# Optimization experiments

Hardware: AMD Instinct MI355X
Metric: run time of the kernel (lower is better)

The kernel has to match this reference:

```python
import jax, jax.numpy as jnp
import numpy as np

N_NODES = 50000
N_EDGES = 800000
NEG_SLOPE = 0.2


def gat_conv(x, W, al, ar, b, src, dst, num_nodes):
    # x: [N, Din]; W: [Din, H*Dout]; al/ar: [H, Dout]; b: [H*Dout]
    H, Dout = al.shape
    h = (x @ W).reshape(num_nodes, H, Dout)            # [N, H, Dout]
    el = jnp.sum(h * al[None], axis=-1)                # [N, H]
    er = jnp.sum(h * ar[None], axis=-1)                # [N, H]
    e = jax.nn.leaky_relu(el[src] + er[dst], NEG_SLOPE)  # [E, H]
    # segment softmax over incoming edges of each dst node
    m = jax.ops.segment_max(e, dst, num_segments=num_nodes)
    m = jnp.where(jnp.isfinite(m), m, 0.0)
    ex = jnp.exp(e - m[dst])                           # [E, H]
    s = jax.ops.segment_sum(ex, dst, num_segments=num_nodes)
    alpha = ex / s[dst]                                # [E, H]
    msg = h[src] * alpha[:, :, None]                   # [E, H, Dout]
    out = jax.ops.segment_sum(msg, dst, num_segments=num_nodes)
    return out + b.reshape(1, H, Dout)                 # [N, H, Dout]


def setup_inputs() -> dict:
    key = jax.random.key(0)
    ks = jax.random.split(key, 12)
    d_in, hid, heads = 128, 128, 2
    inp = {
        "embedding": jax.random.normal(ks[0], (N_NODES, d_in), jnp.float32),
        "W0": jax.random.normal(ks[1], (d_in, heads * hid), jnp.float32) * 0.1,
        "al0": jax.random.normal(ks[2], (heads, hid), jnp.float32) * 0.1,
        "ar0": jax.random.normal(ks[3], (heads, hid), jnp.float32) * 0.1,
        "b0": jnp.zeros((heads * hid,), jnp.float32),
        "W1": jax.random.normal(ks[4], (heads * hid, heads * hid), jnp.float32) * 0.1,
        "al1": jax.random.normal(ks[5], (1, heads * hid), jnp.float32) * 0.1,
        "ar1": jax.random.normal(ks[6], (1, heads * hid), jnp.float32) * 0.1,
        "b1": jnp.zeros((heads * hid,), jnp.float32),
        "src": jax.random.randint(ks[7], (N_EDGES,), 0, N_NODES, jnp.int32),
        "dst": jax.random.randint(ks[8], (N_EDGES,), 0, N_NODES, jnp.int32),
    }
    return inp


def reference(embedding, W0, al0, ar0, b0, W1, al1, ar1, b1, src, dst):
    n = embedding.shape[0]
    # layer 0: 2 heads, then flatten heads and ReLU (dropout no-op in eval)
    x = gat_conv(embedding, W0, al0, ar0, b0, src, dst, n)  # [N, 2, 128]
    x = jax.nn.relu(x.reshape(n, -1))                        # [N, 256]
    # layer 1: 1 head, squeeze
    x = gat_conv(x, W1, al1, ar1, b1, src, dst, n)           # [N, 1, 256]
    x = x.reshape(n, -1)
    x = x.at[0].set(0.0)
    return x
```

## Files before the change

### kernel.cpp

```cpp
#include <hip/hip_runtime.h>


typedef __attribute__((ext_vector_type(8))) short short8v;
typedef __attribute__((ext_vector_type(4))) float f32x4;

__device__ inline unsigned short f2bf(float x) {
    union { float f; unsigned int u; } v; v.f = x;
    unsigned int r = v.u + 0x7fffu + ((v.u >> 16) & 1u);
    return (unsigned short)(r >> 16);
}
__device__ inline float bf2f(unsigned short h) {
    union { unsigned int u; float f; } v; v.u = ((unsigned int)h) << 16;
    return v.f;
}

__global__ void convW(const float* __restrict__ W, unsigned short* __restrict__ Wt,
                      int K, int N)
{
    int t = blockIdx.x * blockDim.x + threadIdx.x;
    if (t < K * N) {
        int k = t / N, n2 = t - k * N;
        Wt[n2 * K + k] = f2bf(W[t]);
    }
}

template<int AFP32, int H>
__global__ __launch_bounds__(256) void gemm_fused(
    const void* __restrict__ Av, const unsigned short* __restrict__ Bt,
    unsigned short* __restrict__ C,
    const float* __restrict__ al, const float* __restrict__ ar,
    float* __restrict__ el, float* __restrict__ er,
    int M, int N, int K)
{
    __shared__ __align__(16) unsigned short As[128 * 64];
    __shared__ __align__(16) unsigned short Bs[64 * 64];
    const int tid = threadIdx.x;
    const int lane = tid & 63, wv = tid >> 6;
    const int rowBase = blockIdx.x * 128;
    const int colBase = blockIdx.y * 64;

    f32x4 acc[2][4];
    #pragma unroll
    for (int i = 0; i < 2; ++i)
        #pragma unroll
        for (int j = 0; j < 4; ++j)
            acc[i][j] = (f32x4){0.f, 0.f, 0.f, 0.f};

    for (int k0 = 0; k0 < K; k0 += 64) {
        #pragma unroll
        for (int c = tid; c < 128 * 8; c += 256) {
            int row = c >> 3, cc = c & 7;
            int gr = rowBase + row; if (gr >= M) gr = M - 1;
            unsigned short* dstp = &As[row * 64 + (cc ^ (row & 7)) * 8];
            if (AFP32) {
                const float* A = (const float*)Av;
                const float* ap = A + (size_t)gr * K + k0 + cc * 8;
                float4 v0 = *(const float4*)ap;
                float4 v1 = *(const float4*)(ap + 4);
                ushort4 o0, o1;
                o0.x = f2bf(v0.x); o0.y = f2bf(v0.y); o0.z = f2bf(v0.z); o0.w = f2bf(v0.w);
                o1.x = f2bf(v1.x); o1.y = f2bf(v1.y); o1.z = f2bf(v1.z); o1.w = f2bf(v1.w);
                *(ushort4*)dstp = o0;
                *(ushort4*)(dstp + 4) = o1;
            } else {
                const unsigned short* A = (const unsigned short*)Av;
                int4 v = *(const int4*)(A + (size_t)gr * K + k0 + cc * 8);
                *(int4*)dstp = v;
            }
        }
        #pragma unroll
        for (int c = tid; c < 64 * 8; c += 256) {
            int n2 = c >> 3, cc = c & 7;
            int4 v = *(const int4*)(Bt + (size_t)(colBase + n2) * K + k0 + cc * 8);
            *(int4*)&Bs[n2 * 64 + (cc ^ (n2 & 7)) * 8] = v;
        }
        __syncthreads();

        #pragma unroll
        for (int ks = 0; ks < 64; ks += 32) {
            int kchunk = (ks >> 3) + (lane >> 4);
            short8v af[2], bfr[4];
            #pragma unroll
            for (int fm = 0; fm < 2; ++fm) {
                int ml = wv * 32 + fm * 16 + (lane & 15);
                af[fm] = *(const short8v*)&As[ml * 64 + (kchunk ^ (ml & 7)) * 8];
            }
            #pragma unroll
            for (int fi = 0; fi < 4; ++fi) {
                int nl = fi * 16 + (lane & 15);
                bfr[fi] = *(const short8v*)&Bs[nl * 64 + (kchunk ^ (nl & 7)) * 8];
            }
            #pragma unroll
            for (int fm = 0; fm < 2; ++fm)
                #pragma unroll
                for (int fi = 0; fi < 4; ++fi)
                    acc[fm][fi] = __builtin_amdgcn_mfma_f32_16x16x32_bf16(
                        af[fm], bfr[fi], acc[fm][fi], 0, 0, 0);
        }
        __syncthreads();
    }

    float alv[4], arv[4];
    #pragma unroll
    for (int fi = 0; fi < 4; ++fi) {
        int col = colBase + fi * 16 + (lane & 15);
        alv[fi] = al[col];
        arv[fi] = ar[col];
    }
    const int head = (H == 2) ? (colBase >> 7) : 0;

    #pragma unroll
    for (int fm = 0; fm < 2; ++fm) {
        #pragma unroll
        for (int r = 0; r < 4; ++r) {
            int row = rowBase + wv * 32 + fm * 16 + (lane >> 4) * 4 + r;
            float pe = acc[fm][0][r] * alv[0] + acc[fm][1][r] * alv[1]
                     + acc[fm][2][r] * alv[2] + acc[fm][3][r] * alv[3];
            float pr2 = acc[fm][0][r] * arv[0] + acc[fm][1][r] * arv[1]
                      + acc[fm][2][r] * arv[2] + acc[fm][3][r] * arv[3];
            #pragma unroll
            for (int off = 8; off; off >>= 1) {
                pe  += __shfl_xor(pe, off);
                pr2 += __shfl_xor(pr2, off);
            }
            if (row < M) {
                #pragma unroll
                for (int fi = 0; fi < 4; ++fi) {
                    int col = colBase + fi * 16 + (lane & 15);
                    C[(size_t)row * N + col] = f2bf(acc[fm][fi][r]);
                }
                if ((lane & 15) == 0) {
                    atomicAdd(&el[row * H + head], pe);
                    atomicAdd(&er[row * H + head], pr2);
                }
            }
        }
    }
}

__global__ void count_kernel(const int* __restrict__ dst, int* __restrict__ cnt, int E)
{
    int t = blockIdx.x * blockDim.x + threadIdx.x;
    if (t < E) atomicAdd(&cnt[dst[t]], 1);
}

__global__ __launch_bounds__(256) void scan_partial(const int* __restrict__ cnt,
                                                    int* __restrict__ bsum, int n)
{
    int t = threadIdx.x;
    int idx = blockIdx.x * 1024 + t * 4;
    int4 v = make_int4(0, 0, 0, 0);
    if (idx + 3 < n) v = *(const int4*)(cnt + idx);
    else if (idx < n) {
        v.x = cnt[idx];
        if (idx + 1 < n) v.y = cnt[idx + 1];
        if (idx + 2 < n) v.z = cnt[idx + 2];
    }
    int s = v.x + v.y + v.z + v.w;
    #pragma unroll
    for (int off = 32; off; off >>= 1) s += __shfl_xor(s, off);
    __shared__ int ws[4];
    if ((t & 63) == 0) ws[t >> 6] = s;
    __syncthreads();
    if (t == 0) bsum[blockIdx.x] = ws[0] + ws[1] + ws[2] + ws[3];
}

__global__ void scan_bsum(int* __restrict__ bsum, int* __restrict__ row,
                          int nb, int n, int E)
{
    int t = threadIdx.x;
    if (nb <= 64) {
        int v = (t < nb) ? bsum[t] : 0;
        int x = v;
        #pragma unroll
        for (int off = 1; off < 64; off <<= 1) {
            int y = __shfl_up(x, off);
            if (t >= off) x += y;
        }
        if (t < nb) bsum[t] = x - v;
    } else if (t == 0) {
        int run = 0;
        for (int i = 0; i < nb; ++i) { int v = bsum[i]; bsum[i] = run; run += v; }
    }
    if (t == 0) row[n] = E;
}

__global__ __launch_bounds__(256) void scan_final(
    const int* __restrict__ cnt, const int* __restrict__ bsum,
    int* __restrict__ row, int* __restrict__ cursor, int n)
{
    int t = threadIdx.x;
    int lane = t & 63;
    int idx = blockIdx.x * 1024 + t * 4;
    int4 v = make_int4(0, 0, 0, 0);
    if (idx + 3 < n) v = *(const int4*)(cnt + idx);
    else if (idx < n) {
        v.x = cnt[idx];
        if (idx + 1 < n) v.y = cnt[idx + 1];
        if (idx + 2 < n) v.z = cnt[idx + 2];
    }
    int s1 = v.x + v.y, s2 = s1 + v.z, s3 = s2 + v.w;
    int tsum = s3;
    int x = tsum;
    #pragma unroll
    for (int off = 1; off < 64; off <<= 1) {
        int y = __shfl_up(x, off);
        if (lane >= off) x += y;
    }
    int wex = x - tsum;
    __shared__ int ws[4];
    if (lane == 63) ws[t >> 6] = x;
    __syncthreads();
    int off0 = bsum[blockIdx.x];
    for (int w2 = 0; w2 < (t >> 6); ++w2) off0 += ws[w2];
    int e0 = off0 + wex;
    if (idx < n)     { row[idx]     = e0;        cursor[idx]     = e0; }
    if (idx + 1 < n) { row[idx + 1] = e0 + v.x;  cursor[idx + 1] = e0 + v.x; }
    if (idx + 2 < n) { row[idx + 2] = e0 + s1;   cursor[idx + 2] = e0 + s1; }
    if (idx + 3 < n) { row[idx + 3] = e0 + s2;   cursor[idx + 3] = e0 + s2; }
}

__global__ void fill_kernel(const int* __restrict__ dst, int* __restrict__ cursor,
                            int* __restrict__ eid, int E)
{
    int t = blockIdx.x * blockDim.x + threadIdx.x;
    if (t < E) {
        int pos = atomicAdd(&cursor[dst[t]], 1);
        eid[pos] = t;
    }
}

template<int H>
__global__ void ecsr_kernel(const int* __restrict__ eid, const int* __restrict__ src,
                            const int* __restrict__ dst, const float* __restrict__ el,
                            const float* __restrict__ er, float* __restrict__ ecsr,
                            int* __restrict__ srcc, int E)
{
    int t = blockIdx.x * blockDim.x + threadIdx.x;
    if (t >= E) return;
    int e = eid[t];
    int s = src[e], d = dst[e];
    srcc[t] = s;
    if (H == 2) {
        float2 l2 = *(const float2*)(el + s * 2);
        float2 r2 = *(const float2*)(er + d * 2);
        float v0 = l2.x + r2.x, v1 = l2.y + r2.y;
        ecsr[t]     = (v0 > 0.f) ? v0 : 0.2f * v0;
        ecsr[E + t] = (v1 > 0.f) ? v1 : 0.2f * v1;
    } else {
        float v = el[s] + er[d];
        ecsr[t] = (v > 0.f) ? v : 0.2f * v;
    }
}

template<int H>
__global__ __launch_bounds__(256) void agg_kernel(
    const unsigned short* __restrict__ h, const float* __restrict__ ecsr,
    const int* __restrict__ srcc, const int* __restrict__ row,
    const float* __restrict__ bias, float* __restrict__ outf,
    unsigned short* __restrict__ outb, int n_nodes, int E,
    int do_relu, int zero0)
{
    int wid = blockIdx.x * 4 + (threadIdx.x >> 6);
    if (wid >= n_nodes) return;
    int lane = threadIdx.x & 63;
    int beg = __builtin_amdgcn_readfirstlane(row[wid]);
    int end = __builtin_amdgcn_readfirstlane(row[wid + 1]);
    const int hsel   = (H == 2) ? (lane >> 5) : 0;
    const int stride = (H == 2) ? 32 : 64;
    const int l0     = (H == 2) ? (lane & 31) : lane;
    const float* plane = ecsr + (size_t)hsel * E;

    float m = -1e30f, s = 0.f;
    for (int i = beg + l0; i < end; i += stride) {
        float ev = plane[i];
        float mn = fmaxf(m, ev);
        s = s * __expf(m - mn) + __expf(ev - mn);
        m = mn;
    }
    #pragma unroll
    for (int off = (H == 2) ? 16 : 32; off; off >>= 1) {
        float mo = __shfl_xor(m, off);
        float so = __shfl_xor(s, off);
        float mn = fmaxf(m, mo);
        s = s * __expf(m - mn) + so * __expf(mo - mn);
        m = mn;
    }
    float r = (s > 0.f) ? 1.f / s : 0.f;

    float aA0 = 0.f, aA1 = 0.f, aA2 = 0.f, aA3 = 0.f;
    float aB0 = 0.f, aB1 = 0.f, aB2 = 0.f, aB3 = 0.f;
    float aC0 = 0.f, aC1 = 0.f, aC2 = 0.f, aC3 = 0.f;
    float aD0 = 0.f, aD1 = 0.f, aD2 = 0.f, aD3 = 0.f;
    int i = beg;
    for (; i + 3 < end; i += 4) {
        float wa = __expf(plane[i]     - m) * r;
        float wb = __expf(plane[i + 1] - m) * r;
        float wc = __expf(plane[i + 2] - m) * r;
        float wd = __expf(plane[i + 3] - m) * r;
        int sa = srcc[i], sb = srcc[i + 1], sc2 = srcc[i + 2], sd = srcc[i + 3];
        ushort4 ha = *(const ushort4*)(h + (size_t)sa * 256 + lane * 4);
        ushort4 hb = *(const ushort4*)(h + (size_t)sb * 256 + lane * 4);
        ushort4 hc = *(const ushort4*)(h + (size_t)sc2 * 256 + lane * 4);
        ushort4 hd = *(const ushort4*)(h + (size_t)sd * 256 + lane * 4);
        aA0 = fmaf(wa, bf2f(ha.x), aA0); aB0 = fmaf(wb, bf2f(hb.x), aB0);
        aC0 = fmaf(wc, bf2f(hc.x), aC0); aD0 = fmaf(wd, bf2f(hd.x), aD0);
        aA1 = fmaf(wa, bf2f(ha.y), aA1); aB1 = fmaf(wb, bf2f(hb.y), aB1);
        aC1 = fmaf(wc, bf2f(hc.y), aC1); aD1 = fmaf(wd, bf2f(hd.y), aD1);
        aA2 = fmaf(wa, bf2f(ha.z), aA2); aB2 = fmaf(wb, bf2f(hb.z), aB2);
        aC2 = fmaf(wc, bf2f(hc.z), aC2); aD2 = fmaf(wd, bf2f(hd.z), aD2);
        aA3 = fmaf(wa, bf2f(ha.w), aA3); aB3 = fmaf(wb, bf2f(hb.w), aB3);
        aC3 = fmaf(wc, bf2f(hc.w), aC3); aD3 = fmaf(wd, bf2f(hd.w), aD3);
    }
    for (; i < end; ++i) {
        float wa = __expf(plane[i] - m) * r;
        int sa = srcc[i];
        ushort4 ha = *(const ushort4*)(h + (size_t)sa * 256 + lane * 4);
        aA0 = fmaf(wa, bf2f(ha.x), aA0);
        aA1 = fmaf(wa, bf2f(ha.y), aA1);
        aA2 = fmaf(wa, bf2f(ha.z), aA2);
        aA3 = fmaf(wa, bf2f(ha.w), aA3);
    }

    float4 b4 = *(const float4*)(bias + lane * 4);
    float o0 = (aA0 + aB0) + (aC0 + aD0) + b4.x;
    float o1 = (aA1 + aB1) + (aC1 + aD1) + b4.y;
    float o2 = (aA2 + aB2) + (aC2 + aD2) + b4.z;
    float o3 = (aA3 + aB3) + (aC3 + aD3) + b4.w;
    if (do_relu) {
        o0 = fmaxf(o0, 0.f); o1 = fmaxf(o1, 0.f);
        o2 = fmaxf(o2, 0.f); o3 = fmaxf(o3, 0.f);
    }
    if (zero0 && wid == 0) { o0 = o1 = o2 = o3 = 0.f; }
    size_t base = (size_t)wid * 256 + lane * 4;
    if (outb) {
        ushort4 o; o.x = f2bf(o0); o.y = f2bf(o1); o.z = f2bf(o2); o.w = f2bf(o3);
        *(ushort4*)(outb + base) = o;
    } else {
        *(float4*)(outf + base) = make_float4(o0, o1, o2, o3);
    }
}

extern "C" void kernel_launch(void* const* d_in, const int* in_sizes, int n_in,
                              void* d_out, int out_size, void* d_ws, size_t ws_size,
                              hipStream_t stream)
{
    const float* emb = (const float*)d_in[0];
    const float* W0  = (const float*)d_in[1];
    const float* al0 = (const float*)d_in[2];
    const float* ar0 = (const float*)d_in[3];
    const float* b0  = (const float*)d_in[4];
    const float* W1  = (const float*)d_in[5];
    const float* al1 = (const float*)d_in[6];
    const float* ar1 = (const float*)d_in[7];
    const float* b1  = (const float*)d_in[8];
    const int* src   = (const int*)d_in[9];
    const int* dst   = (const int*)d_in[10];
    const int N = in_sizes[0] / 128;
    const int E = in_sizes[9];
    float* outp = (float*)d_out;

    char* w = (char*)d_ws;
    auto alloc = [&](size_t bytes) {
        char* p = w;
        w += (bytes + 255) & ~(size_t)255;
        return p;
    };
    unsigned short* hb  = (unsigned short*)alloc((size_t)N * 256 * 2);
    unsigned short* x1b = (unsigned short*)alloc((size_t)N * 256 * 2);
    float* ecsr = (float*)alloc((size_t)E * 2 * 4);
    int* eid    = (int*)alloc((size_t)E * 4);
    int* srcc   = (int*)alloc((size_t)E * 4);
    int* rowp   = (int*)alloc((size_t)(N + 1) * 4);
    float* el   = (float*)alloc((size_t)N * 2 * 4);
    float* er   = (float*)alloc((size_t)N * 2 * 4);
    int* cnt    = (int*)alloc((size_t)N * 4);
    int* cursor = (int*)alloc((size_t)N * 4);
    int* bsum   = (int*)alloc(1024 * 4);
    unsigned short* W0t = (unsigned short*)alloc(256 * 128 * 2);
    unsigned short* W1t = (unsigned short*)alloc(256 * 256 * 2);

    const int nbScan = (N + 1023) / 1024;

    convW<<<(128 * 256 + 255) / 256, 256, 0, stream>>>(W0, W0t, 128, 256);
    convW<<<(256 * 256 + 255) / 256, 256, 0, stream>>>(W1, W1t, 256, 256);

    hipMemsetAsync(cnt, 0, (size_t)N * 4, stream);
    count_kernel<<<(E + 255) / 256, 256, 0, stream>>>(dst, cnt, E);
    scan_partial<<<nbScan, 256, 0, stream>>>(cnt, bsum, N);
    scan_bsum<<<1, 64, 0, stream>>>(bsum, rowp, nbScan, N, E);
    scan_final<<<nbScan, 256, 0, stream>>>(cnt, bsum, rowp, cursor, N);
    fill_kernel<<<(E + 255) / 256, 256, 0, stream>>>(dst, cursor, eid, E);

    hipMemsetAsync(el, 0, (size_t)N * 2 * 4, stream);
    hipMemsetAsync(er, 0, (size_t)N * 2 * 4, stream);
    gemm_fused<1, 2><<<dim3((N + 127) / 128, 4), 256, 0, stream>>>(
        emb, W0t, hb, al0, ar0, el, er, N, 256, 128);
    ecsr_kernel<2><<<(E + 255) / 256, 256, 0, stream>>>(
        eid, src, dst, el, er, ecsr, srcc, E);
    agg_kernel<2><<<(N + 3) / 4, 256, 0, stream>>>(
        hb, ecsr, srcc, rowp, b0, nullptr, x1b, N, E, 1, 0);

    hipMemsetAsync(el, 0, (size_t)N * 4, stream);
    hipMemsetAsync(er, 0, (size_t)N * 4, stream);
    gemm_fused<0, 1><<<dim3((N + 127) / 128, 4), 256, 0, stream>>>(
        x1b, W1t, hb, al1, ar1, el, er, N, 256, 256);
    ecsr_kernel<1><<<(E + 255) / 256, 256, 0, stream>>>(
        eid, src, dst, el, er, ecsr, srcc, E);
    agg_kernel<1><<<(N + 3) / 4, 256, 0, stream>>>(
        hb, ecsr, srcc, rowp, b1, outp, nullptr, N, E, 0, 1);
}
```

Baseline: 318.7 us.

## Store src directly in CSR fill, compute edge scores per node, use exp2 softmax

The fill kernel now writes src ids straight into CSR order, which drops the eid indirection array. Edge-score computation becomes a per-destination-node wave kernel that reads er once per node and gathers el via the CSR src. Scores are pre-scaled by log2(e) so the softmax can use exp2f. The aggregation loop is unrolled to 8 edges to expose more gathers in flight, and the 1/sum normalisation is moved to a single multiply at the end. The per-node kernel may leave lanes idle on nodes with low degree, and the wider unroll raises register use.

```diff
diff --git a/kernel.cpp b/kernel.cpp
--- a/kernel.cpp
+++ b/kernel.cpp
@@ -3,6 +3,8 @@
 
 typedef __attribute__((ext_vector_type(8))) short short8v;
 typedef __attribute__((ext_vector_type(4))) float f32x4;
+
+#define LOG2E 1.4426950408889634f
 
 __device__ inline unsigned short f2bf(float x) {
     union { float f; unsigned int u; } v; v.f = x;
@@ -220,36 +222,41 @@
     if (idx + 3 < n) { row[idx + 3] = e0 + s2;   cursor[idx + 3] = e0 + s2; }
 }
 
-__global__ void fill_kernel(const int* __restrict__ dst, int* __restrict__ cursor,
-                            int* __restrict__ eid, int E)
+__global__ void fill_kernel(const int* __restrict__ src, const int* __restrict__ dst,
+                            int* __restrict__ cursor, int* __restrict__ srcc, int E)
 {
     int t = blockIdx.x * blockDim.x + threadIdx.x;
     if (t < E) {
         int pos = atomicAdd(&cursor[dst[t]], 1);
-        eid[pos] = t;
+        srcc[pos] = src[t];
     }
 }
 
 template<int H>
-__global__ void ecsr_kernel(const int* __restrict__ eid, const int* __restrict__ src,
-                            const int* __restrict__ dst, const float* __restrict__ el,
-                            const float* __restrict__ er, float* __restrict__ ecsr,
-                            int* __restrict__ srcc, int E)
-{
-    int t = blockIdx.x * blockDim.x + threadIdx.x;
-    if (t >= E) return;
-    int e = eid[t];
-    int s = src[e], d = dst[e];
-    srcc[t] = s;
+__global__ __launch_bounds__(256) void ecsr_node(
+    const int* __restrict__ srcc, const int* __restrict__ rowp,
+    const float* __restrict__ el, const float* __restrict__ er,
+    float* __restrict__ ecsr, int n_nodes, int E)
+{
+    int wid = blockIdx.x * 4 + (threadIdx.x >> 6);
+    if (wid >= n_nodes) return;
+    int lane = threadIdx.x & 63;
+    int beg = rowp[wid], end = rowp[wid + 1];
     if (H == 2) {
-        float2 l2 = *(const float2*)(el + s * 2);
-        float2 r2 = *(const float2*)(er + d * 2);
-        float v0 = l2.x + r2.x, v1 = l2.y + r2.y;
-        ecsr[t]     = (v0 > 0.f) ? v0 : 0.2f * v0;
-        ecsr[E + t] = (v1 > 0.f) ? v1 : 0.2f * v1;
+        float2 r2 = *(const float2*)(er + wid * 2);
+        for (int i = beg + lane; i < end; i += 64) {
+            int s = srcc[i];
+            float2 l2 = *(const float2*)(el + s * 2);
+            float v0 = l2.x + r2.x, v1 = l2.y + r2.y;
+            ecsr[i]     = ((v0 > 0.f) ? v0 : 0.2f * v0) * LOG2E;
+            ecsr[E + i] = ((v1 > 0.f) ? v1 : 0.2f * v1) * LOG2E;
+        }
     } else {
-        float v = el[s] + er[d];
-        ecsr[t] = (v > 0.f) ? v : 0.2f * v;
+        float rr = er[wid];
+        for (int i = beg + lane; i < end; i += 64) {
+            float v = el[srcc[i]] + rr;
+            ecsr[i] = ((v > 0.f) ? v : 0.2f * v) * LOG2E;
+        }
     }
 }
 
@@ -275,7 +282,7 @@
     for (int i = beg + l0; i < end; i += stride) {
         float ev = plane[i];
         float mn = fmaxf(m, ev);
-        s = s * __expf(m - mn) + __expf(ev - mn);
+        s = s * exp2f(m - mn) + exp2f(ev - mn);
         m = mn;
     }
     #pragma unroll
@@ -283,7 +290,7 @@
         float mo = __shfl_xor(m, off);
         float so = __shfl_xor(s, off);
         float mn = fmaxf(m, mo);
-        s = s * __expf(m - mn) + so * __expf(mo - mn);
+        s = s * exp2f(m - mn) + so * exp2f(mo - mn);
         m = mn;
     }
     float r = (s > 0.f) ? 1.f / s : 0.f;
@@ -293,11 +300,47 @@
     float aC0 = 0.f, aC1 = 0.f, aC2 = 0.f, aC3 = 0.f;
     float aD0 = 0.f, aD1 = 0.f, aD2 = 0.f, aD3 = 0.f;
     int i = beg;
+    for (; i + 7 < end; i += 8) {
+        float wa = exp2f(plane[i]     - m);
+        float wb = exp2f(plane[i + 1] - m);
+        float wc = exp2f(plane[i + 2] - m);
+        float wd = exp2f(plane[i + 3] - m);
+        float we = exp2f(plane[i + 4] - m);
+        float wf = exp2f(plane[i + 5] - m);
+        float wg = exp2f(plane[i + 6] - m);
+        float wh = exp2f(plane[i + 7] - m);
+        int sa = srcc[i],     sb = srcc[i + 1], sc2 = srcc[i + 2], sd = srcc[i + 3];
+        int se = srcc[i + 4], sf = srcc[i + 5], sg  = srcc[i + 6], sh = srcc[i + 7];
+        ushort4 ha = *(const ushort4*)(h + (size_t)sa * 256 + lane * 4);
+        ushort4 hb = *(const ushort4*)(h + (size_t)sb * 256 + lane * 4);
+        ushort4 hc = *(const ushort4*)(h + (size_t)sc2 * 256 + lane * 4);
+        ushort4 hd = *(const ushort4*)(h + (size_t)sd * 256 + lane * 4);
+        ushort4 he = *(const ushort4*)(h + (size_t)se * 256 + lane * 4);
+        ushort4 hf = *(const ushort4*)(h + (size_t)sf * 256 + lane * 4);
+        ushort4 hg = *(const ushort4*)(h + (size_t)sg * 256 + lane * 4);
+        ushort4 hh = *(const ushort4*)(h + (size_t)sh * 256 + lane * 4);
+        aA0 = fmaf(wa, bf2f(ha.x), aA0); aB0 = fmaf(wb, bf2f(hb.x), aB0);
+        aC0 = fmaf(wc, bf2f(hc.x), aC0); aD0 = fmaf(wd, bf2f(hd.x), aD0);
+        aA1 = fmaf(wa, bf2f(ha.y), aA1); aB1 = fmaf(wb, bf2f(hb.y), aB1);
+        aC1 = fmaf(wc, bf2f(hc.y), aC1); aD1 = fmaf(wd, bf2f(hd.y), aD1);
+        aA2 = fmaf(wa, bf2f(ha.z), aA2); aB2 = fmaf(wb, bf2f(hb.z), aB2);
+        aC2 = fmaf(wc, bf2f(hc.z), aC2); aD2 = fmaf(wd, bf2f(hd.z), aD2);
+        aA3 = fmaf(wa, bf2f(ha.w), aA3); aB3 = fmaf(wb, bf2f(hb.w), aB3);
+        aC3 = fmaf(wc, bf2f(hc.w), aC3); aD3 = fmaf(wd, bf2f(hd.w), aD3);
+        aA0 = fmaf(we, bf2f(he.x), aA0); aB0 = fmaf(wf, bf2f(hf.x), aB0);
+        aC0 = fmaf(wg, bf2f(hg.x), aC0); aD0 = fmaf(wh, bf2f(hh.x), aD0);
+        aA1 = fmaf(we, bf2f(he.y), aA1); aB1 = fmaf(wf, bf2f(hf.y), aB1);
+        aC1 = fmaf(wg, bf2f(hg.y), aC1); aD1 = fmaf(wh, bf2f(hh.y), aD1);
+        aA2 = fmaf(we, bf2f(he.z), aA2); aB2 = fmaf(wf, bf2f(hf.z), aB2);
+        aC2 = fmaf(wg, bf2f(hg.z), aC2); aD2 = fmaf(wh, bf2f(hh.z), aD2);
+        aA3 = fmaf(we, bf2f(he.w), aA3); aB3 = fmaf(wf, bf2f(hf.w), aB3);
+        aC3 = fmaf(wg, bf2f(hg.w), aC3); aD3 = fmaf(wh, bf2f(hh.w), aD3);
+    }
     for (; i + 3 < end; i += 4) {
-        float wa = __expf(plane[i]     - m) * r;
-        float wb = __expf(plane[i + 1] - m) * r;
-        float wc = __expf(plane[i + 2] - m) * r;
-        float wd = __expf(plane[i + 3] - m) * r;
+        float wa = exp2f(plane[i]     - m);
+        float wb = exp2f(plane[i + 1] - m);
+        float wc = exp2f(plane[i + 2] - m);
+        float wd = exp2f(plane[i + 3] - m);
         int sa = srcc[i], sb = srcc[i + 1], sc2 = srcc[i + 2], sd = srcc[i + 3];
         ushort4 ha = *(const ushort4*)(h + (size_t)sa * 256 + lane * 4);
         ushort4 hb = *(const ushort4*)(h + (size_t)sb * 256 + lane * 4);
@@ -313,7 +356,7 @@
         aC3 = fmaf(wc, bf2f(hc.w), aC3); aD3 = fmaf(wd, bf2f(hd.w), aD3);
     }
     for (; i < end; ++i) {
-        float wa = __expf(plane[i] - m) * r;
+        float wa = exp2f(plane[i] - m);
         int sa = srcc[i];
         ushort4 ha = *(const ushort4*)(h + (size_t)sa * 256 + lane * 4);
         aA0 = fmaf(wa, bf2f(ha.x), aA0);
@@ -323,10 +366,10 @@
     }
 
     float4 b4 = *(const float4*)(bias + lane * 4);
-    float o0 = (aA0 + aB0) + (aC0 + aD0) + b4.x;
-    float o1 = (aA1 + aB1) + (aC1 + aD1) + b4.y;
-    float o2 = (aA2 + aB2) + (aC2 + aD2) + b4.z;
-    float o3 = (aA3 + aB3) + (aC3 + aD3) + b4.w;
+    float o0 = ((aA0 + aB0) + (aC0 + aD0)) * r + b4.x;
+    float o1 = ((aA1 + aB1) + (aC1 + aD1)) * r + b4.y;
+    float o2 = ((aA2 + aB2) + (aC2 + aD2)) * r + b4.z;
+    float o3 = ((aA3 + aB3) + (aC3 + aD3)) * r + b4.w;
     if (do_relu) {
         o0 = fmaxf(o0, 0.f); o1 = fmaxf(o1, 0.f);
         o2 = fmaxf(o2, 0.f); o3 = fmaxf(o3, 0.f);
@@ -369,7 +412,6 @@
     unsigned short* hb  = (unsigned short*)alloc((size_t)N * 256 * 2);
     unsigned short* x1b = (unsigned short*)alloc((size_t)N * 256 * 2);
     float* ecsr = (float*)alloc((size_t)E * 2 * 4);
-    int* eid    = (int*)alloc((size_t)E * 4);
     int* srcc   = (int*)alloc((size_t)E * 4);
     int* rowp   = (int*)alloc((size_t)(N + 1) * 4);
     float* el   = (float*)alloc((size_t)N * 2 * 4);
@@ -390,14 +432,13 @@
     scan_partial<<<nbScan, 256, 0, stream>>>(cnt, bsum, N);
     scan_bsum<<<1, 64, 0, stream>>>(bsum, rowp, nbScan, N, E);
     scan_final<<<nbScan, 256, 0, stream>>>(cnt, bsum, rowp, cursor, N);
-    fill_kernel<<<(E + 255) / 256, 256, 0, stream>>>(dst, cursor, eid, E);
+    fill_kernel<<<(E + 255) / 256, 256, 0, stream>>>(src, dst, cursor, srcc, E);
 
     hipMemsetAsync(el, 0, (size_t)N * 2 * 4, stream);
     hipMemsetAsync(er, 0, (size_t)N * 2 * 4, stream);
     gemm_fused<1, 2><<<dim3((N + 127) / 128, 4), 256, 0, stream>>>(
         emb, W0t, hb, al0, ar0, el, er, N, 256, 128);
-    ecsr_kernel<2><<<(E + 255) / 256, 256, 0, stream>>>(
-        eid, src, dst, el, er, ecsr, srcc, E);
+    ecsr_node<2><<<(N + 3) / 4, 256, 0, stream>>>(srcc, rowp, el, er, ecsr, N, E);
     agg_kernel<2><<<(N + 3) / 4, 256, 0, stream>>>(
         hb, ecsr, srcc, rowp, b0, nullptr, x1b, N, E, 1, 0);
 
@@ -405,8 +446,7 @@
     hipMemsetAsync(er, 0, (size_t)N * 4, stream);
     gemm_fused<0, 1><<<dim3((N + 127) / 128, 4), 256, 0, stream>>>(
         x1b, W1t, hb, al1, ar1, el, er, N, 256, 256);
-    ecsr_kernel<1><<<(E + 255) / 256, 256, 0, stream>>>(
-        eid, src, dst, el, er, ecsr, srcc, E);
+    ecsr_node<1><<<(N + 3) / 4, 256, 0, stream>>>(srcc, rowp, el, er, ecsr, N, E);
     agg_kernel<1><<<(N + 3) / 4, 256, 0, stream>>>(
         hb, ecsr, srcc, rowp, b1, outp, nullptr, N, E, 0, 1);
 }
```

New measurement: 315.4 us. About the same (-1.0%).

## Fuse edge-score computation into aggregation and write CSR src directly in fill

Applied to the files above, without the earlier changes.

Removes the separate ecsr_kernel launches per layer. The fill kernel now scatters src indices straight into CSR order instead of edge ids. The aggregation kernel computes leaky-relu scores from el/er in its first pass, stores them pre-scaled by log2(e), and rereads them in the second pass with exp2f. Normalisation by 1/sum moves to the end, and the two weight-conversion kernels merge into one launch. Both passes now run in the same wave, so the stored scores are reread by that wave and a block fence is added between the passes.

```diff
diff --git a/kernel.cpp b/kernel.cpp
--- a/kernel.cpp
+++ b/kernel.cpp
@@ -3,6 +3,8 @@
 
 typedef __attribute__((ext_vector_type(8))) short short8v;
 typedef __attribute__((ext_vector_type(4))) float f32x4;
+
+#define LOG2E 1.4426950408889634f
 
 __device__ inline unsigned short f2bf(float x) {
     union { float f; unsigned int u; } v; v.f = x;
@@ -14,13 +16,18 @@
     return v.f;
 }
 
-__global__ void convW(const float* __restrict__ W, unsigned short* __restrict__ Wt,
-                      int K, int N)
+__global__ void convW_both(const float* __restrict__ W0, unsigned short* __restrict__ W0t,
+                           const float* __restrict__ W1, unsigned short* __restrict__ W1t)
 {
     int t = blockIdx.x * blockDim.x + threadIdx.x;
-    if (t < K * N) {
-        int k = t / N, n2 = t - k * N;
-        Wt[n2 * K + k] = f2bf(W[t]);
+    if (t < 128 * 256) {
+        int k = t >> 8, n2 = t & 255;
+        W0t[n2 * 128 + k] = f2bf(W0[t]);
+    }
+    int u = t - 128 * 256;
+    if (u >= 0 && u < 256 * 256) {
+        int k = u >> 8, n2 = u & 255;
+        W1t[n2 * 256 + k] = f2bf(W1[u]);
     }
 }
 
@@ -220,42 +227,20 @@
     if (idx + 3 < n) { row[idx + 3] = e0 + s2;   cursor[idx + 3] = e0 + s2; }
 }
 
-__global__ void fill_kernel(const int* __restrict__ dst, int* __restrict__ cursor,
-                            int* __restrict__ eid, int E)
+__global__ void fill_kernel(const int* __restrict__ src, const int* __restrict__ dst,
+                            int* __restrict__ cursor, int* __restrict__ srcc, int E)
 {
     int t = blockIdx.x * blockDim.x + threadIdx.x;
     if (t < E) {
         int pos = atomicAdd(&cursor[dst[t]], 1);
-        eid[pos] = t;
-    }
-}
-
-template<int H>
-__global__ void ecsr_kernel(const int* __restrict__ eid, const int* __restrict__ src,
-                            const int* __restrict__ dst, const float* __restrict__ el,
-                            const float* __restrict__ er, float* __restrict__ ecsr,
-                            int* __restrict__ srcc, int E)
-{
-    int t = blockIdx.x * blockDim.x + threadIdx.x;
-    if (t >= E) return;
-    int e = eid[t];
-    int s = src[e], d = dst[e];
-    srcc[t] = s;
-    if (H == 2) {
-        float2 l2 = *(const float2*)(el + s * 2);
-        float2 r2 = *(const float2*)(er + d * 2);
-        float v0 = l2.x + r2.x, v1 = l2.y + r2.y;
-        ecsr[t]     = (v0 > 0.f) ? v0 : 0.2f * v0;
-        ecsr[E + t] = (v1 > 0.f) ? v1 : 0.2f * v1;
-    } else {
-        float v = el[s] + er[d];
-        ecsr[t] = (v > 0.f) ? v : 0.2f * v;
+        srcc[pos] = src[t];
     }
 }
 
 template<int H>
 __global__ __launch_bounds__(256) void agg_kernel(
-    const unsigned short* __restrict__ h, const float* __restrict__ ecsr,
+    const unsigned short* __restrict__ h, const float* __restrict__ el,
+    const float* __restrict__ er, float* __restrict__ ecsr,
     const int* __restrict__ srcc, const int* __restrict__ row,
     const float* __restrict__ bias, float* __restrict__ outf,
     unsigned short* __restrict__ outb, int n_nodes, int E,
@@ -269,13 +254,17 @@
     const int hsel   = (H == 2) ? (lane >> 5) : 0;
     const int stride = (H == 2) ? 32 : 64;
     const int l0     = (H == 2) ? (lane & 31) : lane;
-    const float* plane = ecsr + (size_t)hsel * E;
+    float* plane = ecsr + (size_t)hsel * E;
+    const float rr = er[wid * H + hsel];
 
     float m = -1e30f, s = 0.f;
     for (int i = beg + l0; i < end; i += stride) {
-        float ev = plane[i];
+        int sn = srcc[i];
+        float v = el[sn * H + hsel] + rr;
+        float ev = ((v > 0.f) ? v : 0.2f * v) * LOG2E;
+        plane[i] = ev;
         float mn = fmaxf(m, ev);
-        s = s * __expf(m - mn) + __expf(ev - mn);
+        s = s * exp2f(m - mn) + exp2f(ev - mn);
         m = mn;
     }
     #pragma unroll
@@ -283,10 +272,11 @@
         float mo = __shfl_xor(m, off);
         float so = __shfl_xor(s, off);
         float mn = fmaxf(m, mo);
-        s = s * __expf(m - mn) + so * __expf(mo - mn);
+        s = s * exp2f(m - mn) + so * exp2f(mo - mn);
         m = mn;
     }
     float r = (s > 0.f) ? 1.f / s : 0.f;
+    __threadfence_block();
 
     float aA0 = 0.f, aA1 = 0.f, aA2 = 0.f, aA3 = 0.f;
     float aB0 = 0.f, aB1 = 0.f, aB2 = 0.f, aB3 = 0.f;
@@ -294,10 +284,10 @@
     float aD0 = 0.f, aD1 = 0.f, aD2 = 0.f, aD3 = 0.f;
     int i = beg;
     for (; i + 3 < end; i += 4) {
-        float wa = __expf(plane[i]     - m) * r;
-        float wb = __expf(plane[i + 1] - m) * r;
-        float wc = __expf(plane[i + 2] - m) * r;
-        float wd = __expf(plane[i + 3] - m) * r;
+        float wa = exp2f(plane[i]     - m);
+        float wb = exp2f(plane[i + 1] - m);
+        float wc = exp2f(plane[i + 2] - m);
+        float wd = exp2f(plane[i + 3] - m);
         int sa = srcc[i], sb = srcc[i + 1], sc2 = srcc[i + 2], sd = srcc[i + 3];
         ushort4 ha = *(const ushort4*)(h + (size_t)sa * 256 + lane * 4);
         ushort4 hb = *(const ushort4*)(h + (size_t)sb * 256 + lane * 4);
@@ -313,7 +303,7 @@
         aC3 = fmaf(wc, bf2f(hc.w), aC3); aD3 = fmaf(wd, bf2f(hd.w), aD3);
     }
     for (; i < end; ++i) {
-        float wa = __expf(plane[i] - m) * r;
+        float wa = exp2f(plane[i] - m);
         int sa = srcc[i];
         ushort4 ha = *(const ushort4*)(h + (size_t)sa * 256 + lane * 4);
         aA0 = fmaf(wa, bf2f(ha.x), aA0);
@@ -323,10 +313,10 @@
     }
 
     float4 b4 = *(const float4*)(bias + lane * 4);
-    float o0 = (aA0 + aB0) + (aC0 + aD0) + b4.x;
-    float o1 = (aA1 + aB1) + (aC1 + aD1) + b4.y;
-    float o2 = (aA2 + aB2) + (aC2 + aD2) + b4.z;
-    float o3 = (aA3 + aB3) + (aC3 + aD3) + b4.w;
+    float o0 = ((aA0 + aB0) + (aC0 + aD0)) * r + b4.x;
+    float o1 = ((aA1 + aB1) + (aC1 + aD1)) * r + b4.y;
+    float o2 = ((aA2 + aB2) + (aC2 + aD2)) * r + b4.z;
+    float o3 = ((aA3 + aB3) + (aC3 + aD3)) * r + b4.w;
     if (do_relu) {
         o0 = fmaxf(o0, 0.f); o1 = fmaxf(o1, 0.f);
         o2 = fmaxf(o2, 0.f); o3 = fmaxf(o3, 0.f);
@@ -369,7 +359,6 @@
     unsigned short* hb  = (unsigned short*)alloc((size_t)N * 256 * 2);
     unsigned short* x1b = (unsigned short*)alloc((size_t)N * 256 * 2);
     float* ecsr = (float*)alloc((size_t)E * 2 * 4);
-    int* eid    = (int*)alloc((size_t)E * 4);
     int* srcc   = (int*)alloc((size_t)E * 4);
     int* rowp   = (int*)alloc((size_t)(N + 1) * 4);
     float* el   = (float*)alloc((size_t)N * 2 * 4);
@@ -382,31 +371,27 @@
 
     const int nbScan = (N + 1023) / 1024;
 
-    convW<<<(128 * 256 + 255) / 256, 256, 0, stream>>>(W0, W0t, 128, 256);
-    convW<<<(256 * 256 + 255) / 256, 256, 0, stream>>>(W1, W1t, 256, 256);
+    convW_both<<<(128 * 256 + 256 * 256 + 255) / 256, 256, 0, stream>>>(
+        W0, W0t, W1, W1t);
 
     hipMemsetAsync(cnt, 0, (size_t)N * 4, stream);
     count_kernel<<<(E + 255) / 256, 256, 0, stream>>>(dst, cnt, E);
     scan_partial<<<nbScan, 256, 0, stream>>>(cnt, bsum, N);
     scan_bsum<<<1, 64, 0, stream>>>(bsum, rowp, nbScan, N, E);
     scan_final<<<nbScan, 256, 0, stream>>>(cnt, bsum, rowp, cursor, N);
-    fill_kernel<<<(E + 255) / 256, 256, 0, stream>>>(dst, cursor, eid, E);
+    fill_kernel<<<(E + 255) / 256, 256, 0, stream>>>(src, dst, cursor, srcc, E);
 
     hipMemsetAsync(el, 0, (size_t)N * 2 * 4, stream);
     hipMemsetAsync(er, 0, (size_t)N * 2 * 4, stream);
     gemm_fused<1, 2><<<dim3((N + 127) / 128, 4), 256, 0, stream>>>(
         emb, W0t, hb, al0, ar0, el, er, N, 256, 128);
-    ecsr_kernel<2><<<(E + 255) / 256, 256, 0, stream>>>(
-        eid, src, dst, el, er, ecsr, srcc, E);
     agg_kernel<2><<<(N + 3) / 4, 256, 0, stream>>>(
-        hb, ecsr, srcc, rowp, b0, nullptr, x1b, N, E, 1, 0);
+        hb, el, er, ecsr, srcc, rowp, b0, nullptr, x1b, N, E, 1, 0);
 
     hipMemsetAsync(el, 0, (size_t)N * 4, stream);
     hipMemsetAsync(er, 0, (size_t)N * 4, stream);
     gemm_fused<0, 1><<<dim3((N + 127) / 128, 4), 256, 0, stream>>>(
         x1b, W1t, hb, al1, ar1, el, er, N, 256, 256);
-    ecsr_kernel<1><<<(E + 255) / 256, 256, 0, stream>>>(
-        eid, src, dst, el, er, ecsr, srcc, E);
     agg_kernel<1><<<(N + 3) / 4, 256, 0, stream>>>(
-        hb, ecsr, srcc, rowp, b1, outp, nullptr, N, E, 0, 1);
-}
+        hb, el, er, ecsr, srcc, rowp, b1, outp, nullptr, N, E, 0, 1);
+}
```

Result: faster. 288.0 us (-9.7%).
